# Kernel optimization log

Measured on AMD Instinct MI355X. Metric: run time of the kernel, lower is better.

## Reference

```python
import jax, jax.numpy as jnp
import numpy as np

N, C, T, V = 128, 256, 64, 32
FILTERS = 256

def setup_inputs() -> dict:
    key = jax.random.key(0)
    k1, k2, k3 = jax.random.split(key, 3)
    x = jax.random.normal(k1, (N, C, T, V), dtype=jnp.float32)
    a = jax.random.uniform(k2, (N, T, V, V), dtype=jnp.float32)
    # 1x1 Conv2D (channels_first) == pointwise channel projection: weight [C_in, filters]
    W = jax.random.normal(k3, (C, FILTERS), dtype=jnp.float32) * (2.0 / FILTERS) ** 0.5
    b = jnp.zeros((FILTERS,), dtype=jnp.float32)
    return {"x": x, "a": a, "W": W, "b": b}

def reference(x, a, W, b):
    # 1x1 conv over channels_first input: [n,c,t,v] -> [n,f,t,v]
    h = jnp.einsum('nctv,cf->nftv', x, W) + b[None, :, None, None]
    # Dropout is identity at inference (training=False).
    # Per-frame graph convolution: contract vertex dim with adjacency.
    out = jnp.einsum('nctv,ntvw->nctw', h, a)
    return (out, a)
```

## Files before the change

### kernel.cpp

```cpp
#include <hip/hip_runtime.h>


#define NN 128
#define CC 256
#define TT 64
#define VV 32
#define FF 256
#define TB 4

typedef _Float16 half8 __attribute__((ext_vector_type(8)));
typedef _Float16 half4 __attribute__((ext_vector_type(4)));
typedef float floatx4 __attribute__((ext_vector_type(4)));

__global__ __launch_bounds__(256) void wt_prep_kernel(const float* __restrict__ W,
                                                      _Float16* __restrict__ Wt) {
    const int c = blockIdx.x;
    const int f = threadIdx.x;
    Wt[f * CC + c] = (_Float16)W[c * FF + f];
}

__global__ __launch_bounds__(512, 2) void sgcn_mfma14_kernel(
    const float* __restrict__ x, const float* __restrict__ a,
    const _Float16* __restrict__ Wt, const float* __restrict__ b,
    float* __restrict__ out, float* __restrict__ out_a)
{
    __shared__ _Float16 g_s[TB * VV * 256];
    __shared__ float    s_lds[TB][VV];

    const int tid  = threadIdx.x;
    const int lane = tid & 63;
    const int wv   = tid >> 6;
    const int l15  = lane & 15;
    const int lg   = lane >> 4;
    const int blk  = blockIdx.x;
    const int n    = blk >> 4;
    const int t0   = (blk & 15) * TB;

    char* g_base = (char*)g_s;

    const int tA    = wv >> 1;
    const int chalf = wv & 1;

    const float* a_blk = a + ((size_t)(n * TT + t0)) * (VV * VV);

    float4 xf[16];
    #pragma unroll
    for (int ci = 0; ci < 8; ++ci) {
        const int c = (chalf * 8 + ci) * 16 + l15;
        const float* xp = x + (((size_t)n * CC + c) * TT + (t0 + tA)) * VV + 8 * lg;
        xf[ci * 2 + 0] = *reinterpret_cast<const float4*>(xp);
        xf[ci * 2 + 1] = *reinterpret_cast<const float4*>(xp + 4);
    }

    half8 bA0, bA1;
    {
        const float* at = a_blk + (size_t)tA * (VV * VV);
        #pragma unroll
        for (int j = 0; j < 8; ++j) {
            const float* row = at + (8 * lg + j) * VV;
            bA0[j] = (_Float16)row[l15];
            bA1[j] = (_Float16)row[16 + l15];
        }
    }

    #pragma unroll
    for (int k = 0; k < 2; ++k) {
        const int o = (tid + 512 * k) * 4;
        float4 av = *reinterpret_cast<const float4*>(a_blk + o);
        *reinterpret_cast<float4*>(out_a + ((size_t)(n * TT + t0)) * (VV * VV) + o) = av;
    }

    if (tid < TB * VV) {
        const int it = tid >> 5, w = tid & 31;
        const float* at = a_blk + (size_t)it * (VV * VV) + w;
        float ss = 0.0f;
        #pragma unroll
        for (int v = 0; v < VV; ++v) ss += at[v * VV];
        s_lds[it][w] = ss;
    }

    {
        char* gt = g_base + tA * (VV * 256 * 2);
        #pragma unroll
        for (int ci = 0; ci < 8; ++ci) {
            const int ct = chalf * 8 + ci;
            half8 af;
            float4 x0 = xf[ci * 2 + 0], x1 = xf[ci * 2 + 1];
            af[0] = (_Float16)x0.x; af[1] = (_Float16)x0.y;
            af[2] = (_Float16)x0.z; af[3] = (_Float16)x0.w;
            af[4] = (_Float16)x1.x; af[5] = (_Float16)x1.y;
            af[6] = (_Float16)x1.z; af[7] = (_Float16)x1.w;
            #pragma unroll
            for (int wt = 0; wt < 2; ++wt) {
                floatx4 acc = {0.f, 0.f, 0.f, 0.f};
                acc = __builtin_amdgcn_mfma_f32_16x16x32_f16(af, wt ? bA1 : bA0, acc, 0, 0, 0);
                half4 gh;
                gh[0] = (_Float16)acc[0]; gh[1] = (_Float16)acc[1];
                gh[2] = (_Float16)acc[2]; gh[3] = (_Float16)acc[3];
                const int row = 16 * wt + l15;
                const int cb  = (ct * 16 + 4 * lg) * 2;
                *reinterpret_cast<half4*>(gt + row * 512 + (cb ^ ((row & 7) << 4))) = gh;
            }
        }
    }

    __syncthreads();

    #pragma unroll
    for (int fth = 0; fth < 2; ++fth) {
        const int ft = fth * 8 + wv;
        const int f  = ft * 16 + l15;
        half8 wb[8];
        const _Float16* wp = Wt + (size_t)f * CC + 8 * lg;
        #pragma unroll
        for (int ks = 0; ks < 8; ++ks)
            wb[ks] = *reinterpret_cast<const half8*>(wp + 32 * ks);
        const float bvf = b[f];

        #pragma unroll
        for (int tt = 0; tt < TB; ++tt) {
            char* gt = g_base + tt * (VV * 256 * 2);
            floatx4 acc2[2];
            acc2[0] = (floatx4){0.f, 0.f, 0.f, 0.f};
            acc2[1] = (floatx4){0.f, 0.f, 0.f, 0.f};

            #pragma unroll
            for (int ks = 0; ks < 8; ++ks) {
                const int rr0 = l15, rr1 = 16 + l15;
                const int cb = (32 * ks + 8 * lg) * 2;
                half8 ga0 = *reinterpret_cast<const half8*>(gt + rr0 * 512 +
                                                            (cb ^ ((rr0 & 7) << 4)));
                half8 ga1 = *reinterpret_cast<const half8*>(gt + rr1 * 512 +
                                                            (cb ^ ((rr1 & 7) << 4)));
                acc2[0] = __builtin_amdgcn_mfma_f32_16x16x32_f16(ga0, wb[ks], acc2[0], 0, 0, 0);
                acc2[1] = __builtin_amdgcn_mfma_f32_16x16x32_f16(ga1, wb[ks], acc2[1], 0, 0, 0);
            }

            float* ob = out + (((size_t)n * FF + f) * TT + (t0 + tt)) * VV;
            #pragma unroll
            for (int mt = 0; mt < 2; ++mt) {
                const int w0 = 16 * mt + 4 * lg;
                float4 sv = *reinterpret_cast<const float4*>(&s_lds[tt][w0]);
                float4 o;
                o.x = acc2[mt][0] + bvf * sv.x;
                o.y = acc2[mt][1] + bvf * sv.y;
                o.z = acc2[mt][2] + bvf * sv.z;
                o.w = acc2[mt][3] + bvf * sv.w;
                *reinterpret_cast<float4*>(ob + w0) = o;
            }
        }
    }
}

__global__ __launch_bounds__(256) void sgcn_fused_kernel(
    const float* __restrict__ x, const float* __restrict__ a,
    const float* __restrict__ W, const float* __restrict__ b,
    float* __restrict__ out, float* __restrict__ out_a)
{
    __shared__ float x_lds[CC][VV];
    __shared__ float a_lds[VV][VV];
    const int tid = threadIdx.x;
    const int nt  = blockIdx.x;
    const int n   = nt >> 6;
    const int t   = nt & 63;
    const float* xb = x + (size_t)n * CC * TT * VV + (size_t)t * VV;
    #pragma unroll
    for (int k = 0; k < 8; ++k) {
        int e = tid * 4 + k * 1024;
        int c = e >> 5, v = e & 31;
        float4 val = *reinterpret_cast<const float4*>(xb + (size_t)c * (TT * VV) + v);
        *reinterpret_cast<float4*>(&x_lds[c][v]) = val;
    }
    {
        const float* ab = a + (size_t)nt * (VV * VV);
        float4 av = *reinterpret_cast<const float4*>(ab + tid * 4);
        *reinterpret_cast<float4*>(&a_lds[0][0] + tid * 4) = av;
        *reinterpret_cast<float4*>(out_a + (size_t)nt * (VV * VV) + tid * 4) = av;
    }
    __syncthreads();
    const int f = tid;
    float h[VV];
    #pragma unroll
    for (int v = 0; v < VV; ++v) h[v] = 0.0f;
    #pragma unroll 4
    for (int c = 0; c < CC; ++c) {
        float wv = W[c * FF + f];
        #pragma unroll
        for (int v = 0; v < VV; ++v) h[v] = fmaf(x_lds[c][v], wv, h[v]);
    }
    const float bias = b[f];
    #pragma unroll
    for (int v = 0; v < VV; ++v) h[v] += bias;
    float o[VV];
    #pragma unroll
    for (int w = 0; w < VV; ++w) o[w] = 0.0f;
    #pragma unroll
    for (int v = 0; v < VV; ++v) {
        float hv = h[v];
        #pragma unroll
        for (int w = 0; w < VV; ++w) o[w] = fmaf(hv, a_lds[v][w], o[w]);
    }
    float* ob = out + (((size_t)n * FF + f) * TT + t) * VV;
    #pragma unroll
    for (int w = 0; w < VV; w += 4)
        *reinterpret_cast<float4*>(ob + w) = make_float4(o[w], o[w+1], o[w+2], o[w+3]);
}

extern "C" void kernel_launch(void* const* d_in, const int* in_sizes, int n_in,
                              void* d_out, int out_size, void* d_ws, size_t ws_size,
                              hipStream_t stream) {
    const float* x = (const float*)d_in[0];
    const float* a = (const float*)d_in[1];
    const float* W = (const float*)d_in[2];
    const float* b = (const float*)d_in[3];

    float* out   = (float*)d_out;
    float* out_a = out + (size_t)NN * FF * TT * VV;

    const size_t wt_bytes = (size_t)FF * CC * sizeof(_Float16);

    if (ws_size >= wt_bytes) {
        _Float16* Wt = (_Float16*)d_ws;
        wt_prep_kernel<<<dim3(CC), dim3(FF), 0, stream>>>(W, Wt);
        sgcn_mfma14_kernel<<<dim3(NN * (TT / TB)), dim3(512), 0, stream>>>(x, a, Wt, b, out, out_a);
    } else {
        sgcn_fused_kernel<<<dim3(NN * TT), dim3(256), 0, stream>>>(x, a, W, b, out, out_a);
    }
}
```

Before: 150.4 us.

## Warp-specialize into producer/consumer waves with double-buffered LDS chunks

```diff
diff --git a/kernel.cpp b/kernel.cpp
--- a/kernel.cpp
+++ b/kernel.cpp
@@ -6,7 +6,9 @@
 #define TT 64
 #define VV 32
 #define FF 256
-#define TB 4
+#define TPB 16
+#define TC 2
+#define NCHK 8
 
 typedef _Float16 half8 __attribute__((ext_vector_type(8)));
 typedef _Float16 half4 __attribute__((ext_vector_type(4)));
@@ -19,13 +21,15 @@
     Wt[f * CC + c] = (_Float16)W[c * FF + f];
 }
 
-__global__ __launch_bounds__(512, 2) void sgcn_mfma14_kernel(
+__global__ __launch_bounds__(512, 1) void sgcn_mfma15_kernel(
     const float* __restrict__ x, const float* __restrict__ a,
     const _Float16* __restrict__ Wt, const float* __restrict__ b,
     float* __restrict__ out, float* __restrict__ out_a)
 {
-    __shared__ _Float16 g_s[TB * VV * 256];
-    __shared__ float    s_lds[TB][VV];
+    __shared__ _Float16 g_s[2][TC * VV * 256];
+    __shared__ float    s_slot[2][TC][VV];
+    __shared__ int      ready[2];
+    __shared__ int      done[2];
 
     const int tid  = threadIdx.x;
     const int lane = tid & 63;
@@ -33,121 +37,160 @@
     const int l15  = lane & 15;
     const int lg   = lane >> 4;
     const int blk  = blockIdx.x;
-    const int n    = blk >> 4;
-    const int t0   = (blk & 15) * TB;
-
-    char* g_base = (char*)g_s;
-
-    const int tA    = wv >> 1;
-    const int chalf = wv & 1;
-
-    const float* a_blk = a + ((size_t)(n * TT + t0)) * (VV * VV);
-
-    float4 xf[16];
-    #pragma unroll
-    for (int ci = 0; ci < 8; ++ci) {
-        const int c = (chalf * 8 + ci) * 16 + l15;
-        const float* xp = x + (((size_t)n * CC + c) * TT + (t0 + tA)) * VV + 8 * lg;
-        xf[ci * 2 + 0] = *reinterpret_cast<const float4*>(xp);
-        xf[ci * 2 + 1] = *reinterpret_cast<const float4*>(xp + 4);
-    }
-
-    half8 bA0, bA1;
-    {
-        const float* at = a_blk + (size_t)tA * (VV * VV);
+    const int n    = blk >> 2;
+    const int t0   = (blk & 3) * TPB;
+
+    if (tid < 2) { ready[tid] = 0; done[tid] = 0; }
+    __syncthreads();
+
+    if (wv < 4) {
+        const int tA    = wv >> 1;
+        const int chalf = wv & 1;
+
+        #pragma unroll 1
+        for (int ch = 0; ch < NCHK; ++ch) {
+            const int slot  = ch & 1;
+            const int round = ch >> 1;
+            while (__hip_atomic_load(&done[slot], __ATOMIC_ACQUIRE,
+                                     __HIP_MEMORY_SCOPE_WORKGROUP) < 4 * round)
+                __builtin_amdgcn_s_sleep(1);
+
+            const int tch = t0 + ch * TC;
+            const int t   = tch + tA;
+
+            float4 xf[16];
+            #pragma unroll
+            for (int ci = 0; ci < 8; ++ci) {
+                const int c = (chalf * 8 + ci) * 16 + l15;
+                const float* xp = x + (((size_t)n * CC + c) * TT + t) * VV + 8 * lg;
+                xf[ci * 2 + 0] = *reinterpret_cast<const float4*>(xp);
+                xf[ci * 2 + 1] = *reinterpret_cast<const float4*>(xp + 4);
+            }
+
+            half8 bA0, bA1;
+            float ps0 = 0.0f, ps1 = 0.0f;
+            {
+                const float* at = a + (size_t)(n * TT + t) * (VV * VV);
+                #pragma unroll
+                for (int j = 0; j < 8; ++j) {
+                    const float* row = at + (8 * lg + j) * VV;
+                    const float e0 = row[l15];
+                    const float e1 = row[16 + l15];
+                    bA0[j] = (_Float16)e0;
+                    bA1[j] = (_Float16)e1;
+                    ps0 += e0;
+                    ps1 += e1;
+                }
+            }
+            ps0 += __shfl_xor(ps0, 16); ps0 += __shfl_xor(ps0, 32);
+            ps1 += __shfl_xor(ps1, 16); ps1 += __shfl_xor(ps1, 32);
+            if (chalf == 0 && lane < 16) {
+                s_slot[slot][tA][lane]      = ps0;
+                s_slot[slot][tA][16 + lane] = ps1;
+            }
+
+            {
+                const float* ab = a + (size_t)(n * TT + tch) * (VV * VV);
+                float* ob = out_a + (size_t)(n * TT + tch) * (VV * VV);
+                float4 m0 = *reinterpret_cast<const float4*>(ab + tid * 4);
+                float4 m1 = *reinterpret_cast<const float4*>(ab + tid * 4 + 1024);
+                *reinterpret_cast<float4*>(ob + tid * 4)        = m0;
+                *reinterpret_cast<float4*>(ob + tid * 4 + 1024) = m1;
+            }
+
+            char* gt = (char*)&g_s[slot][0] + tA * (VV * 256 * 2);
+            #pragma unroll
+            for (int ci = 0; ci < 8; ++ci) {
+                const int ct = chalf * 8 + ci;
+                half8 af;
+                float4 x0 = xf[ci * 2 + 0], x1 = xf[ci * 2 + 1];
+                af[0] = (_Float16)x0.x; af[1] = (_Float16)x0.y;
+                af[2] = (_Float16)x0.z; af[3] = (_Float16)x0.w;
+                af[4] = (_Float16)x1.x; af[5] = (_Float16)x1.y;
+                af[6] = (_Float16)x1.z; af[7] = (_Float16)x1.w;
+                #pragma unroll
+                for (int wt = 0; wt < 2; ++wt) {
+                    floatx4 acc = {0.f, 0.f, 0.f, 0.f};
+                    acc = __builtin_amdgcn_mfma_f32_16x16x32_f16(af, wt ? bA1 : bA0, acc, 0, 0, 0);
+                    half4 gh;
+                    gh[0] = (_Float16)acc[0]; gh[1] = (_Float16)acc[1];
+                    gh[2] = (_Float16)acc[2]; gh[3] = (_Float16)acc[3];
+                    const int row = 16 * wt + l15;
+                    const int cb  = (ct * 16 + 4 * lg) * 2;
+                    *reinterpret_cast<half4*>(gt + row * 512 + (cb ^ ((row & 7) << 4))) = gh;
+                }
+            }
+
+            asm volatile("" ::: "memory");
+            if (lane == 0)
+                __hip_atomic_fetch_add(&ready[slot], 1, __ATOMIC_RELEASE,
+                                       __HIP_MEMORY_SCOPE_WORKGROUP);
+        }
+    } else {
+        const int cw = wv - 4;
+
+        half8 wb[32];
+        float bvf[4];
         #pragma unroll
-        for (int j = 0; j < 8; ++j) {
-            const float* row = at + (8 * lg + j) * VV;
-            bA0[j] = (_Float16)row[l15];
-            bA1[j] = (_Float16)row[16 + l15];
+        for (int fth = 0; fth < 4; ++fth) {
+            const int f = (cw + 4 * fth) * 16 + l15;
+            const _Float16* wp = Wt + (size_t)f * CC + 8 * lg;
+            #pragma unroll
+            for (int ks = 0; ks < 8; ++ks)
+                wb[fth * 8 + ks] = *reinterpret_cast<const half8*>(wp + 32 * ks);
+            bvf[fth] = b[f];
         }
-    }
-
-    #pragma unroll
-    for (int k = 0; k < 2; ++k) {
-        const int o = (tid + 512 * k) * 4;
-        float4 av = *reinterpret_cast<const float4*>(a_blk + o);
-        *reinterpret_cast<float4*>(out_a + ((size_t)(n * TT + t0)) * (VV * VV) + o) = av;
-    }
-
-    if (tid < TB * VV) {
-        const int it = tid >> 5, w = tid & 31;
-        const float* at = a_blk + (size_t)it * (VV * VV) + w;
-        float ss = 0.0f;
-        #pragma unroll
-        for (int v = 0; v < VV; ++v) ss += at[v * VV];
-        s_lds[it][w] = ss;
-    }
-
-    {
-        char* gt = g_base + tA * (VV * 256 * 2);
-        #pragma unroll
-        for (int ci = 0; ci < 8; ++ci) {
-            const int ct = chalf * 8 + ci;
-            half8 af;
-            float4 x0 = xf[ci * 2 + 0], x1 = xf[ci * 2 + 1];
-            af[0] = (_Float16)x0.x; af[1] = (_Float16)x0.y;
-            af[2] = (_Float16)x0.z; af[3] = (_Float16)x0.w;
-            af[4] = (_Float16)x1.x; af[5] = (_Float16)x1.y;
-            af[6] = (_Float16)x1.z; af[7] = (_Float16)x1.w;
-            #pragma unroll
-            for (int wt = 0; wt < 2; ++wt) {
-                floatx4 acc = {0.f, 0.f, 0.f, 0.f};
-                acc = __builtin_amdgcn_mfma_f32_16x16x32_f16(af, wt ? bA1 : bA0, acc, 0, 0, 0);
-                half4 gh;
-                gh[0] = (_Float16)acc[0]; gh[1] = (_Float16)acc[1];
-                gh[2] = (_Float16)acc[2]; gh[3] = (_Float16)acc[3];
-                const int row = 16 * wt + l15;
-                const int cb  = (ct * 16 + 4 * lg) * 2;
-                *reinterpret_cast<half4*>(gt + row * 512 + (cb ^ ((row & 7) << 4))) = gh;
-            }
-        }
-    }
-
-    __syncthreads();
-
-    #pragma unroll
-    for (int fth = 0; fth < 2; ++fth) {
-        const int ft = fth * 8 + wv;
-        const int f  = ft * 16 + l15;
-        half8 wb[8];
-        const _Float16* wp = Wt + (size_t)f * CC + 8 * lg;
-        #pragma unroll
-        for (int ks = 0; ks < 8; ++ks)
-            wb[ks] = *reinterpret_cast<const half8*>(wp + 32 * ks);
-        const float bvf = b[f];
-
-        #pragma unroll
-        for (int tt = 0; tt < TB; ++tt) {
-            char* gt = g_base + tt * (VV * 256 * 2);
-            floatx4 acc2[2];
-            acc2[0] = (floatx4){0.f, 0.f, 0.f, 0.f};
-            acc2[1] = (floatx4){0.f, 0.f, 0.f, 0.f};
-
-            #pragma unroll
-            for (int ks = 0; ks < 8; ++ks) {
-                const int rr0 = l15, rr1 = 16 + l15;
-                const int cb = (32 * ks + 8 * lg) * 2;
-                half8 ga0 = *reinterpret_cast<const half8*>(gt + rr0 * 512 +
-                                                            (cb ^ ((rr0 & 7) << 4)));
-                half8 ga1 = *reinterpret_cast<const half8*>(gt + rr1 * 512 +
-                                                            (cb ^ ((rr1 & 7) << 4)));
-                acc2[0] = __builtin_amdgcn_mfma_f32_16x16x32_f16(ga0, wb[ks], acc2[0], 0, 0, 0);
-                acc2[1] = __builtin_amdgcn_mfma_f32_16x16x32_f16(ga1, wb[ks], acc2[1], 0, 0, 0);
-            }
-
-            float* ob = out + (((size_t)n * FF + f) * TT + (t0 + tt)) * VV;
-            #pragma unroll
-            for (int mt = 0; mt < 2; ++mt) {
-                const int w0 = 16 * mt + 4 * lg;
-                float4 sv = *reinterpret_cast<const float4*>(&s_lds[tt][w0]);
-                float4 o;
-                o.x = acc2[mt][0] + bvf * sv.x;
-                o.y = acc2[mt][1] + bvf * sv.y;
-                o.z = acc2[mt][2] + bvf * sv.z;
-                o.w = acc2[mt][3] + bvf * sv.w;
-                *reinterpret_cast<float4*>(ob + w0) = o;
-            }
+
+        #pragma unroll 1
+        for (int ch = 0; ch < NCHK; ++ch) {
+            const int slot   = ch & 1;
+            const int target = 4 * ((ch >> 1) + 1);
+            while (__hip_atomic_load(&ready[slot], __ATOMIC_ACQUIRE,
+                                     __HIP_MEMORY_SCOPE_WORKGROUP) < target)
+                __builtin_amdgcn_s_sleep(1);
+
+            const int tch = t0 + ch * TC;
+            #pragma unroll
+            for (int fth = 0; fth < 4; ++fth) {
+                const int f = (cw + 4 * fth) * 16 + l15;
+                #pragma unroll
+                for (int tt = 0; tt < TC; ++tt) {
+                    char* gt = (char*)&g_s[slot][0] + tt * (VV * 256 * 2);
+                    floatx4 acc2[2];
+                    acc2[0] = (floatx4){0.f, 0.f, 0.f, 0.f};
+                    acc2[1] = (floatx4){0.f, 0.f, 0.f, 0.f};
+
+                    #pragma unroll
+                    for (int ks = 0; ks < 8; ++ks) {
+                        const int rr0 = l15, rr1 = 16 + l15;
+                        const int cb = (32 * ks + 8 * lg) * 2;
+                        half8 ga0 = *reinterpret_cast<const half8*>(gt + rr0 * 512 +
+                                                                    (cb ^ ((rr0 & 7) << 4)));
+                        half8 ga1 = *reinterpret_cast<const half8*>(gt + rr1 * 512 +
+                                                                    (cb ^ ((rr1 & 7) << 4)));
+                        acc2[0] = __builtin_amdgcn_mfma_f32_16x16x32_f16(ga0, wb[fth * 8 + ks], acc2[0], 0, 0, 0);
+                        acc2[1] = __builtin_amdgcn_mfma_f32_16x16x32_f16(ga1, wb[fth * 8 + ks], acc2[1], 0, 0, 0);
+                    }
+
+                    float* ob = out + (((size_t)n * FF + f) * TT + (tch + tt)) * VV;
+                    #pragma unroll
+                    for (int mt = 0; mt < 2; ++mt) {
+                        const int w0 = 16 * mt + 4 * lg;
+                        float4 sv = *reinterpret_cast<const float4*>(&s_slot[slot][tt][w0]);
+                        float4 o;
+                        o.x = acc2[mt][0] + bvf[fth] * sv.x;
+                        o.y = acc2[mt][1] + bvf[fth] * sv.y;
+                        o.z = acc2[mt][2] + bvf[fth] * sv.z;
+                        o.w = acc2[mt][3] + bvf[fth] * sv.w;
+                        *reinterpret_cast<float4*>(ob + w0) = o;
+                    }
+                }
+            }
+
+            asm volatile("" ::: "memory");
+            if (lane == 0)
+                __hip_atomic_fetch_add(&done[slot], 1, __ATOMIC_RELEASE,
+                                       __HIP_MEMORY_SCOPE_WORKGROUP);
         }
     }
 }
@@ -222,7 +265,7 @@
     if (ws_size >= wt_bytes) {
         _Float16* Wt = (_Float16*)d_ws;
         wt_prep_kernel<<<dim3(CC), dim3(FF), 0, stream>>>(W, Wt);
-        sgcn_mfma14_kernel<<<dim3(NN * (TT / TB)), dim3(512), 0, stream>>>(x, a, Wt, b, out, out_a);
+        sgcn_mfma15_kernel<<<dim3(NN * (TT / TPB)), dim3(512), 0, stream>>>(x, a, Wt, b, out, out_a);
     } else {
         sgcn_fused_kernel<<<dim3(NN * TT), dim3(256), 0, stream>>>(x, a, W, b, out, out_a);
     }
```

Result: faster. 147.3 us (-2.1%).
